# Optimization experiments

Measured on AMD Instinct MI355X. Metric: run time of the kernel, lower is better.

The kernel has to match this reference:

```python
import jax, jax.numpy as jnp
import numpy as np

TOKENS, IN_F, OUT_F = 8192, 4096, 4096

def setup_inputs() -> dict:
    key = jax.random.key(0)
    k1, k2, k3, k4 = jax.random.split(key, 4)
    # int8 activations and weights in [-127, 127]
    x = jax.random.randint(k1, (TOKENS, IN_F), -127, 128, dtype=jnp.int32).astype(jnp.int8)
    weight = jax.random.randint(k2, (OUT_F, IN_F), -127, 128, dtype=jnp.int32).astype(jnp.int8)  # [out, in]
    # static per-output-channel dequant scale (fp16), small so fp16 output doesn't overflow
    dequant_scale = (jax.random.uniform(k3, (OUT_F,), dtype=jnp.float32) * 1e-3).astype(jnp.float16)
    bias = (jax.random.normal(k4, (OUT_F,), dtype=jnp.float32)).astype(jnp.float16)
    return {"x": x, "weight": weight, "dequant_scale": dequant_scale, "bias": bias}

def reference(x, weight, dequant_scale, bias):
    # int8 GEMM with int32 accumulation: [tokens, in] @ [in, out] -> [tokens, out]
    acc = jax.lax.dot_general(
        x, weight.T,
        dimension_numbers=(((1,), (0,)), ((), ())),
        preferred_element_type=jnp.int32,
    )
    # static per-output-channel dequant, cast to fp16, add fp16 bias
    out = (acc.astype(jnp.float32) * dequant_scale.astype(jnp.float32)[None, :]).astype(jnp.float16)
    out = out + bias[None, :]
    # module returns (output, output_bias)
    return (out, bias)
```

## Files before the change

kernel.cpp:

```cpp
#include <hip/hip_runtime.h>
#include <hip/hip_fp16.h>
#include <stdint.h>

typedef __attribute__((ext_vector_type(4))) int int32x4;
typedef __attribute__((ext_vector_type(4))) float float32x4;

#define TOKENS 8192
#define IN_F   4096
#define OUT_F  4096
#define BM 256
#define BN 256
#define BK 128
#define NT (IN_F / BK)
#define ESTR 260

#define AS1 __attribute__((address_space(1)))
#define AS3 __attribute__((address_space(3)))

__global__ __launch_bounds__(256)
void pack_all_kernel(const int* __restrict__ x32, const int* __restrict__ w32,
                     const float* __restrict__ bias,
                     uint32_t* __restrict__ x8, uint32_t* __restrict__ w8,
                     float* __restrict__ bias_out)
{
    const int gid = blockIdx.x * 256 + threadIdx.x;
    if (gid < OUT_F / 4) {
        float32x4 b4 = __builtin_nontemporal_load((const float32x4*)bias + gid);
        __builtin_nontemporal_store(b4, (float32x4*)bias_out + gid);
    }

    const int nx4 = TOKENS * IN_F / 4;
    const int nw4 = OUT_F * IN_F / 4;
    for (int i = gid; i < nx4 + nw4; i += gridDim.x * 256) {
        const int* s; uint32_t* d; int j;
        if (i < nx4) { s = x32; d = x8; j = i; }
        else         { s = w32; d = w8; j = i - nx4; }
        int32x4 v = __builtin_nontemporal_load((const int32x4*)s + j);
        d[j] = (uint32_t)(v[0] & 0xff) | ((uint32_t)(v[1] & 0xff) << 8) |
               ((uint32_t)(v[2] & 0xff) << 16) | ((uint32_t)v[3] << 24);
    }
}

__global__ __launch_bounds__(512, 2)
void w8a8_gemm_kernel(const int8_t* __restrict__ x,
                      const int8_t* __restrict__ w,
                      const float* __restrict__ scale,
                      const float* __restrict__ bias,
                      float* __restrict__ out)
{
    __shared__ int8_t smem[131072];
    int8_t* lA = smem;
    int8_t* lB = smem + 65536;

    const int tid = threadIdx.x;
    const int wv  = tid >> 6;
    const int l   = tid & 63;
    const int wqm = wv >> 1;
    const int wqn = wv & 1;

    const int xc  = blockIdx.x & 7;
    const int idx = blockIdx.x >> 3;
    const int bn  = (xc & 1) * 8 + (idx & 7);
    const int bm  = (xc >> 1) * 8 + (idx >> 3);

    const int8_t* baseA = x + (size_t)bm * BM * IN_F;
    const int8_t* baseB = w + (size_t)bn * BN * IN_F;

    const int seg0 = wv * 2, seg1 = wv * 2 + 1;
    const int r8   = l >> 3;
    const int swc  = (((l & 7) ^ r8) << 4);

    const int8_t* pA0 = baseA + (size_t)(seg0 * 8 + r8) * IN_F + swc;
    const int8_t* pA1 = baseA + (size_t)(seg1 * 8 + r8) * IN_F + swc;
    const int8_t* pB0 = baseB + (size_t)(seg0 * 8 + r8) * IN_F + swc;
    const int8_t* pB1 = baseB + (size_t)(seg1 * 8 + r8) * IN_F + swc;

    const int fr  = l & 15;
    const int xk  = (l & 7) << 4;
    const int cb0 = (l >> 4) << 4;

    int32x4 acc[2][2][2][4];
#pragma unroll
    for (int a0 = 0; a0 < 2; ++a0)
#pragma unroll
        for (int a1 = 0; a1 < 2; ++a1)
#pragma unroll
            for (int a2 = 0; a2 < 2; ++a2)
#pragma unroll
                for (int a3 = 0; a3 < 4; ++a3)
                    acc[a0][a1][a2][a3] = (int32x4){0, 0, 0, 0};

    int32x4 aF[2][2];
    int32x4 bF0[4][2];
    int32x4 bF1[4][2];

    auto stage_half = [&](int h4) {
        const int kt_ = h4 >> 2;
        const int wh_ = h4 & 3;
        const size_t off = (size_t)(wh_ & 1) * (128 * IN_F) + (size_t)kt_ * BK;
        const int8_t* s0 = ((wh_ < 2) ? pA0 : pB0) + off;
        const int8_t* s1 = ((wh_ < 2) ? pA1 : pB1) + off;
        int8_t* db = ((wh_ < 2) ? lA : lB) + ((kt_ & 1) << 15) + ((wh_ & 1) << 14);
        __builtin_amdgcn_global_load_lds(
            (const AS1 void*)s0, (AS3 void*)(db + seg0 * 1024), 16, 0, 0);
        __builtin_amdgcn_global_load_lds(
            (const AS1 void*)s1, (AS3 void*)(db + seg1 * 1024), 16, 0, 0);
    };

#define LDA(MH)                                                                        \
    do {                                                                               \
        _Pragma("unroll") for (int mi = 0; mi < 2; ++mi)                               \
        _Pragma("unroll") for (int ks = 0; ks < 2; ++ks)                               \
            aF[mi][ks] = *(const int32x4*)&lAb[((MH) << 14) +                          \
                (wqm * 32 + mi * 16 + fr) * 128 + (((ks * 64) + cb0) ^ xk)];           \
    } while (0)

#define LDB(NH, DST)                                                                   \
    do {                                                                               \
        _Pragma("unroll") for (int ni = 0; ni < 4; ++ni)                               \
        _Pragma("unroll") for (int ks = 0; ks < 2; ++ks)                               \
            DST[ni][ks] = *(const int32x4*)&lBb[((NH) << 14) +                         \
                (wqn * 64 + ni * 16 + fr) * 128 + (((ks * 64) + cb0) ^ xk)];           \
    } while (0)

#define MMAQ(MH, NH, BF)                                                               \
    do {                                                                               \
        _Pragma("unroll") for (int mi = 0; mi < 2; ++mi)                               \
        _Pragma("unroll") for (int ni = 0; ni < 4; ++ni)                               \
        _Pragma("unroll") for (int ks = 0; ks < 2; ++ks)                               \
            acc[MH][NH][mi][ni] = __builtin_amdgcn_mfma_i32_16x16x64_i8(               \
                aF[mi][ks], BF[ni][ks], acc[MH][NH][mi][ni], 0, 0, 0);                 \
    } while (0)

    stage_half(0); stage_half(1); stage_half(2); stage_half(3);
    stage_half(4);
    asm volatile("s_waitcnt vmcnt(2)" ::: "memory");
    __builtin_amdgcn_s_barrier();

    for (int t = 0; t < NT; ++t) {
        const int8_t* lAb = lA + ((t & 1) << 15);
        const int8_t* lBb = lB + ((t & 1) << 15);

        LDA(0); LDB(0, bF0); LDB(1, bF1);
        if (t + 1 < NT) {
            stage_half(4 * (t + 1) + 1);
            stage_half(4 * (t + 1) + 2);
            stage_half(4 * (t + 1) + 3);
        }
        __builtin_amdgcn_s_barrier();
        asm volatile("s_waitcnt lgkmcnt(0)" ::: "memory");
        __builtin_amdgcn_s_setprio(1);
        MMAQ(0, 0, bF0); MMAQ(0, 1, bF1);
        __builtin_amdgcn_s_setprio(0);
        __builtin_amdgcn_s_barrier();

        LDA(1);
        if (t + 2 < NT) stage_half(4 * (t + 2) + 0);
        if (t + 2 < NT)      asm volatile("s_waitcnt vmcnt(2)" ::: "memory");
        else if (t + 1 < NT) asm volatile("s_waitcnt vmcnt(0)" ::: "memory");
        __builtin_amdgcn_s_barrier();
        asm volatile("s_waitcnt lgkmcnt(0)" ::: "memory");
        __builtin_amdgcn_s_setprio(1);
        MMAQ(1, 0, bF0); MMAQ(1, 1, bF1);
        __builtin_amdgcn_s_setprio(0);
        __builtin_amdgcn_s_barrier();
    }

    __syncthreads();
    int* eL = (int*)smem;
    const int c4   = tid & 63;
    const int rowt = tid >> 6;
    const float32x4 sc4 = ((const float32x4*)scale)[bn * 64 + c4];
    const float32x4 bf4 = ((const float32x4*)bias )[bn * 64 + c4];
    const __half bh[4] = { __float2half(bf4[0]), __float2half(bf4[1]),
                           __float2half(bf4[2]), __float2half(bf4[3]) };
    const int r0 = (l >> 4) << 2;
    const int wr0 = (wqm & 1) * 32 + r0;

    for (int c = 0; c < 4; ++c) {
        if ((wqm >> 1) == (c & 1)) {
            const int MH = c >> 1;
#pragma unroll
            for (int NH = 0; NH < 2; ++NH)
#pragma unroll
                for (int mi = 0; mi < 2; ++mi)
#pragma unroll
                    for (int ni = 0; ni < 4; ++ni)
#pragma unroll
                        for (int r = 0; r < 4; ++r)
                            eL[(wr0 + mi * 16 + r) * ESTR +
                               NH * 128 + wqn * 64 + ni * 16 + fr] = acc[MH][NH][mi][ni][r];
        }
        __syncthreads();
#pragma unroll
        for (int p = 0; p < 8; ++p) {
            const int rl = p * 8 + rowt;
            int32x4 v = *(const int32x4*)&eL[rl * ESTR + c4 * 4];
            float32x4 o;
#pragma unroll
            for (int j = 0; j < 4; ++j) {
                __half h = __float2half((float)v[j] * sc4[j]);
                o[j] = __half2float(__hadd(h, bh[j]));
            }
            const size_t rowg = (size_t)(bm * 256 + c * 64 + rl);
            __builtin_nontemporal_store(o, (float32x4*)out + rowg * (OUT_F / 4) + bn * 64 + c4);
        }
        __syncthreads();
    }
#undef LDA
#undef LDB
#undef MMAQ
}

extern "C" void kernel_launch(void* const* d_in, const int* in_sizes, int n_in,
                              void* d_out, int out_size, void* d_ws, size_t ws_size,
                              hipStream_t stream)
{
    const int*   x32   = (const int*)d_in[0];
    const int*   w32   = (const int*)d_in[1];
    const float* scale = (const float*)d_in[2];
    const float* bias  = (const float*)d_in[3];
    float* out = (float*)d_out;

    int8_t* x8 = (int8_t*)d_ws;
    int8_t* w8 = x8 + (size_t)TOKENS * IN_F;

    pack_all_kernel<<<3072, 256, 0, stream>>>(x32, w32, bias, (uint32_t*)x8, (uint32_t*)w8,
                                              out + (size_t)TOKENS * OUT_F);

    w8a8_gemm_kernel<<<512, 512, 0, stream>>>(x8, w8, scale, bias, out);
}
```

Before: 189.1 us.

## Simplify main loop to single-phase load-all, prefetch-next, compute-all schedule

Replaces the two-phase ping-pong main loop, which used staggered half-tile prefetches and several barriers per iteration, with a simpler schedule. Each iteration now loads all A and B fragments, issues the whole next tile's global-to-LDS copies, runs all MFMAs, then waits for vmcnt(0) and takes one barrier. This cuts barriers and keeps A fragments for both halves live at once, so register pressure rises. It also waits for the whole next tile at the end of each iteration, which can leave less global-load latency hidden than the staggered prefetch did.

```diff
diff --git a/kernel.cpp b/kernel.cpp
--- a/kernel.cpp
+++ b/kernel.cpp
@@ -90,9 +90,8 @@
                 for (int a3 = 0; a3 < 4; ++a3)
                     acc[a0][a1][a2][a3] = (int32x4){0, 0, 0, 0};
 
-    int32x4 aF[2][2];
-    int32x4 bF0[4][2];
-    int32x4 bF1[4][2];
+    int32x4 aF[2][2][2];
+    int32x4 bF[2][4][2];
 
     auto stage_half = [&](int h4) {
         const int kt_ = h4 >> 2;
@@ -111,58 +110,47 @@
     do {                                                                               \
         _Pragma("unroll") for (int mi = 0; mi < 2; ++mi)                               \
         _Pragma("unroll") for (int ks = 0; ks < 2; ++ks)                               \
-            aF[mi][ks] = *(const int32x4*)&lAb[((MH) << 14) +                          \
+            aF[MH][mi][ks] = *(const int32x4*)&lAb[((MH) << 14) +                      \
                 (wqm * 32 + mi * 16 + fr) * 128 + (((ks * 64) + cb0) ^ xk)];           \
     } while (0)
 
-#define LDB(NH, DST)                                                                   \
+#define LDB(NH)                                                                        \
     do {                                                                               \
         _Pragma("unroll") for (int ni = 0; ni < 4; ++ni)                               \
         _Pragma("unroll") for (int ks = 0; ks < 2; ++ks)                               \
-            DST[ni][ks] = *(const int32x4*)&lBb[((NH) << 14) +                         \
+            bF[NH][ni][ks] = *(const int32x4*)&lBb[((NH) << 14) +                      \
                 (wqn * 64 + ni * 16 + fr) * 128 + (((ks * 64) + cb0) ^ xk)];           \
     } while (0)
 
-#define MMAQ(MH, NH, BF)                                                               \
+#define MMAQ(MH, NH)                                                                   \
     do {                                                                               \
         _Pragma("unroll") for (int mi = 0; mi < 2; ++mi)                               \
         _Pragma("unroll") for (int ni = 0; ni < 4; ++ni)                               \
         _Pragma("unroll") for (int ks = 0; ks < 2; ++ks)                               \
             acc[MH][NH][mi][ni] = __builtin_amdgcn_mfma_i32_16x16x64_i8(               \
-                aF[mi][ks], BF[ni][ks], acc[MH][NH][mi][ni], 0, 0, 0);                 \
+                aF[MH][mi][ks], bF[NH][ni][ks], acc[MH][NH][mi][ni], 0, 0, 0);         \
     } while (0)
 
     stage_half(0); stage_half(1); stage_half(2); stage_half(3);
-    stage_half(4);
-    asm volatile("s_waitcnt vmcnt(2)" ::: "memory");
+    asm volatile("s_waitcnt vmcnt(0)" ::: "memory");
     __builtin_amdgcn_s_barrier();
 
     for (int t = 0; t < NT; ++t) {
         const int8_t* lAb = lA + ((t & 1) << 15);
         const int8_t* lBb = lB + ((t & 1) << 15);
 
-        LDA(0); LDB(0, bF0); LDB(1, bF1);
+        LDA(0); LDB(0); LDB(1); LDA(1);
+
         if (t + 1 < NT) {
-            stage_half(4 * (t + 1) + 1);
-            stage_half(4 * (t + 1) + 2);
-            stage_half(4 * (t + 1) + 3);
+            stage_half(4 * (t + 1) + 0); stage_half(4 * (t + 1) + 1);
+            stage_half(4 * (t + 1) + 2); stage_half(4 * (t + 1) + 3);
         }
-        __builtin_amdgcn_s_barrier();
-        asm volatile("s_waitcnt lgkmcnt(0)" ::: "memory");
+
         __builtin_amdgcn_s_setprio(1);
-        MMAQ(0, 0, bF0); MMAQ(0, 1, bF1);
+        MMAQ(0, 0); MMAQ(0, 1); MMAQ(1, 0); MMAQ(1, 1);
         __builtin_amdgcn_s_setprio(0);
-        __builtin_amdgcn_s_barrier();
-
-        LDA(1);
-        if (t + 2 < NT) stage_half(4 * (t + 2) + 0);
-        if (t + 2 < NT)      asm volatile("s_waitcnt vmcnt(2)" ::: "memory");
-        else if (t + 1 < NT) asm volatile("s_waitcnt vmcnt(0)" ::: "memory");
-        __builtin_amdgcn_s_barrier();
-        asm volatile("s_waitcnt lgkmcnt(0)" ::: "memory");
-        __builtin_amdgcn_s_setprio(1);
-        MMAQ(1, 0, bF0); MMAQ(1, 1, bF1);
-        __builtin_amdgcn_s_setprio(0);
+
+        if (t + 1 < NT) asm volatile("s_waitcnt vmcnt(0)" ::: "memory");
         __builtin_amdgcn_s_barrier();
     }
 
```

Result: no change. 185.9 us (-1.7%).
